# Kernel tuning notes

Measured on AMD Instinct MI355X. Metric: run time of the kernel, lower is better.

The kernel has to match this reference:

```python
import jax, jax.numpy as jnp
import numpy as np

NUM_HEAD = 12
D_MODEL = 768
SEQ_LEN = 4096
D_K = D_MODEL // NUM_HEAD
NEG = -1e9  # matches masked_fill(-1000000000.0)


def setup_inputs() -> dict:
    key = jax.random.key(0)
    ks = jax.random.split(key, 9)
    s = 1.0 / np.sqrt(D_MODEL)
    inp = {
        "x": jax.random.normal(ks[0], (1, SEQ_LEN, D_MODEL), jnp.float32),
        "Wq": jax.random.normal(ks[1], (D_MODEL, D_MODEL), jnp.float32) * s,
        "bq": jax.random.normal(ks[2], (D_MODEL,), jnp.float32) * 0.01,
        "Wk": jax.random.normal(ks[3], (D_MODEL, D_MODEL), jnp.float32) * s,
        "bk": jax.random.normal(ks[4], (D_MODEL,), jnp.float32) * 0.01,
        "Wv": jax.random.normal(ks[5], (D_MODEL, D_MODEL), jnp.float32) * s,
        "bv": jax.random.normal(ks[6], (D_MODEL,), jnp.float32) * 0.01,
        "Wo": jax.random.normal(ks[7], (D_MODEL, D_MODEL), jnp.float32) * s,
        "bo": jax.random.normal(ks[8], (D_MODEL,), jnp.float32) * 0.01,
    }
    return inp


def reference(x, Wq, bq, Wk, bk, Wv, bv, Wo, bo):
    # x: [B, S, D]. nn.Linear computes x @ W.T + b.
    B, S, D = x.shape

    def proj(W, b):
        y = jnp.einsum("bsd,ed->bse", x, W) + b
        # [B, S, H, d_k] -> [B, H, S, d_k]
        return y.reshape(B, S, NUM_HEAD, D_K).transpose(0, 2, 1, 3)

    q = proj(Wq, bq)
    k = proj(Wk, bk)
    v = proj(Wv, bv)

    scores = jnp.einsum("bhqd,bhkd->bhqk", q, k) / jnp.sqrt(
        jnp.asarray(D_K, x.dtype)
    )
    # causal (subsequent) mask: position q attends to k <= q
    causal = jnp.tril(jnp.ones((S, S), bool))
    scores = jnp.where(causal[None, None], scores, jnp.asarray(NEG, x.dtype))
    p_attn = jax.nn.softmax(scores, axis=-1)  # dropout is identity in eval
    ctx = jnp.einsum("bhqk,bhkd->bhqd", p_attn, v)
    ctx = ctx.transpose(0, 2, 1, 3).reshape(B, S, D)
    return jnp.einsum("bsd,ed->bse", ctx, Wo) + bo
```

## Files before the change

kernel.cpp:

```cpp
#include <hip/hip_runtime.h>

#define SEQ 4096
#define DM  768
#define NH  12
#define DK  64

typedef __bf16 bf16_t;
typedef bf16_t bf16x8 __attribute__((ext_vector_type(8)));
typedef bf16_t bf16x4 __attribute__((ext_vector_type(4)));
typedef float  f32x4  __attribute__((ext_vector_type(4)));
typedef short  s16x4  __attribute__((ext_vector_type(4)));

#define LOG2E 1.44269504088896340736f
#define SM_C  16.0f

static __device__ inline f32x4 mfma16x16x16_bf16(bf16x4 a, bf16x4 b, f32x4 c) {
#if __has_builtin(__builtin_amdgcn_mfma_f32_16x16x16_bf16)
    return __builtin_amdgcn_mfma_f32_16x16x16_bf16(a, b, c, 0, 0, 0);
#else
    return __builtin_amdgcn_mfma_f32_16x16x16bf16_1k(
        __builtin_bit_cast(s16x4, a), __builtin_bit_cast(s16x4, b), c, 0, 0, 0);
#endif
}

__global__ __launch_bounds__(256) void gemm_qkv(
    const float* __restrict__ x,
    const float* __restrict__ Wq, const float* __restrict__ bq,
    const float* __restrict__ Wk, const float* __restrict__ bk,
    const float* __restrict__ Wv, const float* __restrict__ bv,
    bf16_t* __restrict__ Qb, bf16_t* __restrict__ Kb, bf16_t* __restrict__ Vbt)
{
    const float* W; const float* bias;
    if (blockIdx.z == 0)      { W = Wq; bias = bq; }
    else if (blockIdx.z == 1) { W = Wk; bias = bk; }
    else                      { W = Wv; bias = bv; }

    __shared__ bf16_t As[128][40];
    __shared__ bf16_t Bs[128][40];

    const int tid  = threadIdx.x;
    const int wave = tid >> 6;
    const int lane = tid & 63;
    const int wm   = wave & 1, wn = wave >> 1;
    const int lrow = lane & 15;
    const int quad = lane >> 4;
    const int row0 = blockIdx.x * 128;
    const int col0 = blockIdx.y * 128;

    f32x4 acc[4][4];
    #pragma unroll
    for (int i = 0; i < 4; i++)
        #pragma unroll
        for (int j = 0; j < 4; j++)
            acc[i][j] = (f32x4){0.f, 0.f, 0.f, 0.f};

    for (int k0 = 0; k0 < DM; k0 += 32) {
        __syncthreads();
        #pragma unroll
        for (int i = 0; i < 4; i++) {
            int v  = tid + i * 256;
            int r  = v >> 3;
            int c4 = v & 7;
            float4 av = *(const float4*)&x[(size_t)(row0 + r) * DM + k0 + c4 * 4];
            bf16x4 at;
            at[0] = (bf16_t)av.x; at[1] = (bf16_t)av.y;
            at[2] = (bf16_t)av.z; at[3] = (bf16_t)av.w;
            *(bf16x4*)&As[r][c4 * 4] = at;
            float4 bv4 = *(const float4*)&W[(size_t)(col0 + r) * DM + k0 + c4 * 4];
            bf16x4 bt;
            bt[0] = (bf16_t)bv4.x; bt[1] = (bf16_t)bv4.y;
            bt[2] = (bf16_t)bv4.z; bt[3] = (bf16_t)bv4.w;
            *(bf16x4*)&Bs[r][c4 * 4] = bt;
        }
        __syncthreads();

        bf16x8 afrag[4], bfrag[4];
        #pragma unroll
        for (int mt = 0; mt < 4; mt++)
            afrag[mt] = *(const bf16x8*)&As[wm * 64 + mt * 16 + lrow][quad * 8];
        #pragma unroll
        for (int nt = 0; nt < 4; nt++)
            bfrag[nt] = *(const bf16x8*)&Bs[wn * 64 + nt * 16 + lrow][quad * 8];
        #pragma unroll
        for (int mt = 0; mt < 4; mt++)
            #pragma unroll
            for (int nt = 0; nt < 4; nt++)
                acc[mt][nt] = __builtin_amdgcn_mfma_f32_16x16x32_bf16(
                    afrag[mt], bfrag[nt], acc[mt][nt], 0, 0, 0);
    }

    if (blockIdx.z == 2) {
        #pragma unroll
        for (int nt = 0; nt < 4; nt++) {
            int col = col0 + wn * 64 + nt * 16 + lrow;
            float bv = bias[col];
            #pragma unroll
            for (int mt = 0; mt < 4; mt++) {
                int row = row0 + wm * 64 + mt * 16 + quad * 4;
                bf16x4 t;
                #pragma unroll
                for (int r = 0; r < 4; r++) t[r] = (bf16_t)(acc[mt][nt][r] + bv);
                *(bf16x4*)&Vbt[(size_t)col * SEQ + row] = t;
            }
        }
    } else {
        bf16_t* Cout = (blockIdx.z == 0) ? Qb : Kb;
        #pragma unroll
        for (int nt = 0; nt < 4; nt++) {
            int col = col0 + wn * 64 + nt * 16 + lrow;
            float bv = bias[col];
            #pragma unroll
            for (int mt = 0; mt < 4; mt++) {
                #pragma unroll
                for (int r = 0; r < 4; r++) {
                    int row = row0 + wm * 64 + mt * 16 + quad * 4 + r;
                    Cout[(size_t)row * DM + col] = (bf16_t)(acc[mt][nt][r] + bv);
                }
            }
        }
    }
}

__global__ __launch_bounds__(256) void gemm_out(
    const bf16_t* __restrict__ A, const float* __restrict__ W,
    const float* __restrict__ bias, float* __restrict__ C)
{
    __shared__ bf16_t As[128][40];
    __shared__ bf16_t Bs[128][40];

    const int tid  = threadIdx.x;
    const int wave = tid >> 6;
    const int lane = tid & 63;
    const int wm   = wave & 1, wn = wave >> 1;
    const int lrow = lane & 15;
    const int quad = lane >> 4;
    const int row0 = blockIdx.x * 128;
    const int col0 = blockIdx.y * 128;

    f32x4 acc[4][4];
    #pragma unroll
    for (int i = 0; i < 4; i++)
        #pragma unroll
        for (int j = 0; j < 4; j++)
            acc[i][j] = (f32x4){0.f, 0.f, 0.f, 0.f};

    for (int k0 = 0; k0 < DM; k0 += 32) {
        __syncthreads();
        #pragma unroll
        for (int i = 0; i < 2; i++) {
            int v  = tid + i * 256;
            int r  = v >> 2;
            int c8 = v & 3;
            *(bf16x8*)&As[r][c8 * 8] =
                *(const bf16x8*)&A[(size_t)(row0 + r) * DM + k0 + c8 * 8];
        }
        #pragma unroll
        for (int i = 0; i < 4; i++) {
            int v  = tid + i * 256;
            int r  = v >> 3;
            int c4 = v & 7;
            float4 bv4 = *(const float4*)&W[(size_t)(col0 + r) * DM + k0 + c4 * 4];
            bf16x4 bt;
            bt[0] = (bf16_t)bv4.x; bt[1] = (bf16_t)bv4.y;
            bt[2] = (bf16_t)bv4.z; bt[3] = (bf16_t)bv4.w;
            *(bf16x4*)&Bs[r][c4 * 4] = bt;
        }
        __syncthreads();

        bf16x8 afrag[4], bfrag[4];
        #pragma unroll
        for (int mt = 0; mt < 4; mt++)
            afrag[mt] = *(const bf16x8*)&As[wm * 64 + mt * 16 + lrow][quad * 8];
        #pragma unroll
        for (int nt = 0; nt < 4; nt++)
            bfrag[nt] = *(const bf16x8*)&Bs[wn * 64 + nt * 16 + lrow][quad * 8];
        #pragma unroll
        for (int mt = 0; mt < 4; mt++)
            #pragma unroll
            for (int nt = 0; nt < 4; nt++)
                acc[mt][nt] = __builtin_amdgcn_mfma_f32_16x16x32_bf16(
                    afrag[mt], bfrag[nt], acc[mt][nt], 0, 0, 0);
    }

    #pragma unroll
    for (int nt = 0; nt < 4; nt++) {
        int col = col0 + wn * 64 + nt * 16 + lrow;
        float bv = bias[col];
        #pragma unroll
        for (int mt = 0; mt < 4; mt++) {
            #pragma unroll
            for (int r = 0; r < 4; r++) {
                int row = row0 + wm * 64 + mt * 16 + quad * 4 + r;
                C[(size_t)row * DM + col] = acc[mt][nt][r] + bv;
            }
        }
    }
}

__global__ __launch_bounds__(256) void flash_attn(
    const bf16_t* __restrict__ Qb, const bf16_t* __restrict__ Kb,
    const bf16_t* __restrict__ Vbt, bf16_t* __restrict__ Ctx)
{
    const int qi   = gridDim.x - 1 - blockIdx.x;
    const int h    = blockIdx.y;
    const int tid  = threadIdx.x;
    const int wave = tid >> 6;
    const int lane = tid & 63;
    const int lrow = lane & 15;
    const int quad = lane >> 4;
    const int q0   = qi * 64;

    __shared__ bf16_t Ks[64][72];
    __shared__ bf16_t Vt[64][76];

    const int qrow = q0 + wave * 16 + lrow;
    bf16x8 qfrag[2];
    #pragma unroll
    for (int s = 0; s < 2; s++) {
        bf16x8 t = *(const bf16x8*)&Qb[(size_t)qrow * DM + h * DK + s * 32 + quad * 8];
        #pragma unroll
        for (int j = 0; j < 8; j++)
            t[j] = (bf16_t)((float)t[j] * 0.125f);
        qfrag[s] = t;
    }

    f32x4 oT[4];
    #pragma unroll
    for (int dt = 0; dt < 4; dt++) oT[dt] = (f32x4){0.f, 0.f, 0.f, 0.f};
    float l_i = 0.f;

    const int r0 = tid >> 3;
    const int c0 = (tid & 7) * 8;

    const bf16_t* Kbase = Kb  + (size_t)h * DK + c0;
    const bf16_t* Vbase = Vbt + (size_t)(h * DK) * SEQ + c0;

    bf16x8 kr0 = *(const bf16x8*)&Kbase[(size_t)(r0)      * DM];
    bf16x8 kr1 = *(const bf16x8*)&Kbase[(size_t)(r0 + 32) * DM];
    bf16x8 vr0 = *(const bf16x8*)&Vbase[(size_t)(r0)      * SEQ];
    bf16x8 vr1 = *(const bf16x8*)&Vbase[(size_t)(r0 + 32) * SEQ];

    for (int kt = 0; kt <= qi; kt++) {
        __syncthreads();
        *(bf16x8*)&Ks[r0][c0]      = kr0;
        *(bf16x8*)&Ks[r0 + 32][c0] = kr1;
        *(bf16x8*)&Vt[r0][c0]      = vr0;
        *(bf16x8*)&Vt[r0 + 32][c0] = vr1;
        __syncthreads();

        if (kt < qi) {
            size_t ko = (size_t)(kt + 1) * 64;
            kr0 = *(const bf16x8*)&Kbase[(ko + r0)      * DM];
            kr1 = *(const bf16x8*)&Kbase[(ko + r0 + 32) * DM];
            vr0 = *(const bf16x8*)&Vbase[(size_t)(r0)      * SEQ + ko];
            vr1 = *(const bf16x8*)&Vbase[(size_t)(r0 + 32) * SEQ + ko];
        }

        f32x4 sc[4];
        #pragma unroll
        for (int mt = 0; mt < 4; mt++) {
            f32x4 a = (f32x4){0.f, 0.f, 0.f, 0.f};
            #pragma unroll
            for (int s = 0; s < 2; s++) {
                bf16x8 kf = *(const bf16x8*)&Ks[mt * 16 + lrow][s * 32 + quad * 8];
                a = __builtin_amdgcn_mfma_f32_16x16x32_bf16(kf, qfrag[s], a, 0, 0, 0);
            }
            sc[mt] = a;
        }

        if (kt == qi) {
            int lq = wave * 16 + lrow;
            #pragma unroll
            for (int mt = 0; mt < 4; mt++)
                #pragma unroll
                for (int r = 0; r < 4; r++)
                    if (mt * 16 + quad * 4 + r > lq) sc[mt][r] = -1e30f;
        }

        bf16x4 pf[4];
        float rsum = 0.f;
        #pragma unroll
        for (int mt = 0; mt < 4; mt++) {
            bf16x4 t;
            #pragma unroll
            for (int r = 0; r < 4; r++) {
                float p = __builtin_amdgcn_exp2f((sc[mt][r] - SM_C) * LOG2E);
                rsum += p;
                t[r] = (bf16_t)p;
            }
            pf[mt] = t;
        }
        l_i += rsum;

        #pragma unroll
        for (int dt = 0; dt < 4; dt++)
            #pragma unroll
            for (int kb = 0; kb < 4; kb++) {
                bf16x4 vf = *(const bf16x4*)&Vt[dt * 16 + lrow][kb * 16 + quad * 4];
                oT[dt] = mfma16x16x16_bf16(vf, pf[kb], oT[dt]);
            }
    }

    l_i += __shfl_xor(l_i, 16, 64);
    l_i += __shfl_xor(l_i, 32, 64);
    float inv_l = 1.f / l_i;
    #pragma unroll
    for (int dt = 0; dt < 4; dt++) {
        bf16x4 ov;
        #pragma unroll
        for (int r = 0; r < 4; r++) ov[r] = (bf16_t)(oT[dt][r] * inv_l);
        *(bf16x4*)&Ctx[(size_t)(q0 + wave * 16 + lrow) * DM
                       + h * DK + dt * 16 + quad * 4] = ov;
    }
}

extern "C" void kernel_launch(void* const* d_in, const int* in_sizes, int n_in,
                              void* d_out, int out_size, void* d_ws, size_t ws_size,
                              hipStream_t stream) {
    const float* x  = (const float*)d_in[0];
    const float* Wq = (const float*)d_in[1];
    const float* bq = (const float*)d_in[2];
    const float* Wk = (const float*)d_in[3];
    const float* bk = (const float*)d_in[4];
    const float* Wv = (const float*)d_in[5];
    const float* bv = (const float*)d_in[6];
    const float* Wo = (const float*)d_in[7];
    const float* bo = (const float*)d_in[8];
    float* out = (float*)d_out;

    bf16_t* Qb  = (bf16_t*)d_ws;
    bf16_t* Kb  = Qb  + (size_t)SEQ * DM;
    bf16_t* Vbt = Kb  + (size_t)SEQ * DM;
    bf16_t* Cx  = Vbt + (size_t)SEQ * DM;

    dim3 g1(SEQ / 128, DM / 128, 3);
    gemm_qkv<<<g1, 256, 0, stream>>>(x, Wq, bq, Wk, bk, Wv, bv, Qb, Kb, Vbt);

    dim3 g2(SEQ / 64, NH);
    flash_attn<<<g2, 256, 0, stream>>>(Qb, Kb, Vbt, Cx);

    dim3 g3(SEQ / 128, DM / 128);
    gemm_out<<<g3, 256, 0, stream>>>(Cx, Wo, bo, out);
}
```

Measured before the change: 232.3 us.

## Pre-convert to bf16, use direct LDS loads, and split attention over key chunks

Adds a conversion kernel that turns x and all weights into bf16 once, so the GEMMs can stream bf16 through global_load_lds into XOR-swizzled 64-wide K tiles. The attention kernel is split along the key axis into up to four 16-tile chunks with double-buffered LDS and no per-tile barrier pair; partial outputs and row sums are accumulated with float atomics, then normalized and transposed in a new epilogue kernel. The Q scale moves into K's projection epilogue, and the output GEMM uses 128x64 tiles for more blocks. The split is meant to fix load imbalance from the causal triangle, but it adds a memset, atomic traffic, a fixed softmax offset shared across chunks, and two extra launches.

```diff
diff --git a/kernel.cpp b/kernel.cpp
--- a/kernel.cpp
+++ b/kernel.cpp
@@ -23,20 +23,48 @@
 #endif
 }
 
-__global__ __launch_bounds__(256) void gemm_qkv(
-    const float* __restrict__ x,
-    const float* __restrict__ Wq, const float* __restrict__ bq,
-    const float* __restrict__ Wk, const float* __restrict__ bk,
-    const float* __restrict__ Wv, const float* __restrict__ bv,
+static __device__ __forceinline__ void gl_lds16(const bf16_t* g, bf16_t* l) {
+    __builtin_amdgcn_global_load_lds(
+        (const __attribute__((address_space(1))) void*)g,
+        (__attribute__((address_space(3))) void*)l, 16, 0, 0);
+}
+
+__global__ __launch_bounds__(256) void cvt_bf16(
+    const float* __restrict__ x,  const float* __restrict__ Wq,
+    const float* __restrict__ Wk, const float* __restrict__ Wv,
+    const float* __restrict__ Wo,
+    bf16_t* __restrict__ xb, bf16_t* __restrict__ Wb)
+{
+    const int NXV = SEQ * DM / 4;
+    const int NWV = DM * DM / 4;
+    int i4 = blockIdx.x * 256 + threadIdx.x;
+    const float* src; bf16_t* dst; int off;
+    if (i4 < NXV) { src = x; dst = xb; off = i4; }
+    else {
+        int j = i4 - NXV;
+        int w = j / NWV, jj = j - w * NWV;
+        src = (w == 0) ? Wq : (w == 1) ? Wk : (w == 2) ? Wv : Wo;
+        dst = Wb + (size_t)w * DM * DM;
+        off = jj;
+    }
+    float4 v = *(const float4*)&src[(size_t)off * 4];
+    bf16x4 t;
+    t[0] = (bf16_t)v.x; t[1] = (bf16_t)v.y; t[2] = (bf16_t)v.z; t[3] = (bf16_t)v.w;
+    *(bf16x4*)&dst[(size_t)off * 4] = t;
+}
+
+__global__ __launch_bounds__(256) void gemm_qkv2(
+    const bf16_t* __restrict__ A, const bf16_t* __restrict__ Wb,
+    const float* __restrict__ bq, const float* __restrict__ bk,
+    const float* __restrict__ bv,
     bf16_t* __restrict__ Qb, bf16_t* __restrict__ Kb, bf16_t* __restrict__ Vbt)
 {
-    const float* W; const float* bias;
-    if (blockIdx.z == 0)      { W = Wq; bias = bq; }
-    else if (blockIdx.z == 1) { W = Wk; bias = bk; }
-    else                      { W = Wv; bias = bv; }
-
-    __shared__ bf16_t As[128][40];
-    __shared__ bf16_t Bs[128][40];
+    const int z = blockIdx.z;
+    const bf16_t* W = Wb + (size_t)z * DM * DM;
+    const float* bias = (z == 0) ? bq : (z == 1) ? bk : bv;
+
+    __shared__ bf16_t As[128][64];
+    __shared__ bf16_t Bs[128][64];
 
     const int tid  = threadIdx.x;
     const int wave = tid >> 6;
@@ -47,6 +75,10 @@
     const int row0 = blockIdx.x * 128;
     const int col0 = blockIdx.y * 128;
 
+    const int srow   = lane >> 3;
+    const int schunk = (lane & 7) ^ srow;
+    const int swz    = lrow & 7;
+
     f32x4 acc[4][4];
     #pragma unroll
     for (int i = 0; i < 4; i++)
@@ -54,79 +86,78 @@
         for (int j = 0; j < 4; j++)
             acc[i][j] = (f32x4){0.f, 0.f, 0.f, 0.f};
 
-    for (int k0 = 0; k0 < DM; k0 += 32) {
+    for (int k0 = 0; k0 < DM; k0 += 64) {
         __syncthreads();
         #pragma unroll
-        for (int i = 0; i < 4; i++) {
-            int v  = tid + i * 256;
-            int r  = v >> 3;
-            int c4 = v & 7;
-            float4 av = *(const float4*)&x[(size_t)(row0 + r) * DM + k0 + c4 * 4];
-            bf16x4 at;
-            at[0] = (bf16_t)av.x; at[1] = (bf16_t)av.y;
-            at[2] = (bf16_t)av.z; at[3] = (bf16_t)av.w;
-            *(bf16x4*)&As[r][c4 * 4] = at;
-            float4 bv4 = *(const float4*)&W[(size_t)(col0 + r) * DM + k0 + c4 * 4];
-            bf16x4 bt;
-            bt[0] = (bf16_t)bv4.x; bt[1] = (bf16_t)bv4.y;
-            bt[2] = (bf16_t)bv4.z; bt[3] = (bf16_t)bv4.w;
-            *(bf16x4*)&Bs[r][c4 * 4] = bt;
+        for (int u = 0; u < 4; u++) {
+            int R0 = wave * 32 + u * 8;
+            gl_lds16(&A[(size_t)(row0 + R0 + srow) * DM + k0 + schunk * 8],
+                     &As[R0][0]);
+            gl_lds16(&W[(size_t)(col0 + R0 + srow) * DM + k0 + schunk * 8],
+                     &Bs[R0][0]);
         }
         __syncthreads();
 
-        bf16x8 afrag[4], bfrag[4];
-        #pragma unroll
-        for (int mt = 0; mt < 4; mt++)
-            afrag[mt] = *(const bf16x8*)&As[wm * 64 + mt * 16 + lrow][quad * 8];
-        #pragma unroll
-        for (int nt = 0; nt < 4; nt++)
-            bfrag[nt] = *(const bf16x8*)&Bs[wn * 64 + nt * 16 + lrow][quad * 8];
-        #pragma unroll
-        for (int mt = 0; mt < 4; mt++)
+        #pragma unroll
+        for (int s = 0; s < 2; s++) {
+            bf16x8 af[4], bfr[4];
+            #pragma unroll
+            for (int mt = 0; mt < 4; mt++)
+                af[mt] = *(const bf16x8*)
+                    &As[wm * 64 + mt * 16 + lrow][(((s << 2) | quad) ^ swz) * 8];
             #pragma unroll
             for (int nt = 0; nt < 4; nt++)
-                acc[mt][nt] = __builtin_amdgcn_mfma_f32_16x16x32_bf16(
-                    afrag[mt], bfrag[nt], acc[mt][nt], 0, 0, 0);
-    }
-
-    if (blockIdx.z == 2) {
+                bfr[nt] = *(const bf16x8*)
+                    &Bs[wn * 64 + nt * 16 + lrow][(((s << 2) | quad) ^ swz) * 8];
+            #pragma unroll
+            for (int mt = 0; mt < 4; mt++)
+                #pragma unroll
+                for (int nt = 0; nt < 4; nt++)
+                    acc[mt][nt] = __builtin_amdgcn_mfma_f32_16x16x32_bf16(
+                        af[mt], bfr[nt], acc[mt][nt], 0, 0, 0);
+        }
+    }
+
+    if (z == 2) {
         #pragma unroll
         for (int nt = 0; nt < 4; nt++) {
             int col = col0 + wn * 64 + nt * 16 + lrow;
-            float bv = bias[col];
+            float bvv = bias[col];
             #pragma unroll
             for (int mt = 0; mt < 4; mt++) {
                 int row = row0 + wm * 64 + mt * 16 + quad * 4;
                 bf16x4 t;
                 #pragma unroll
-                for (int r = 0; r < 4; r++) t[r] = (bf16_t)(acc[mt][nt][r] + bv);
+                for (int r = 0; r < 4; r++) t[r] = (bf16_t)(acc[mt][nt][r] + bvv);
                 *(bf16x4*)&Vbt[(size_t)col * SEQ + row] = t;
             }
         }
     } else {
-        bf16_t* Cout = (blockIdx.z == 0) ? Qb : Kb;
+        bf16_t* Cout = (z == 0) ? Qb : Kb;
+        float scale = (z == 1) ? 0.125f : 1.0f;
         #pragma unroll
         for (int nt = 0; nt < 4; nt++) {
             int col = col0 + wn * 64 + nt * 16 + lrow;
-            float bv = bias[col];
+            float bvv = bias[col];
             #pragma unroll
             for (int mt = 0; mt < 4; mt++) {
                 #pragma unroll
                 for (int r = 0; r < 4; r++) {
                     int row = row0 + wm * 64 + mt * 16 + quad * 4 + r;
-                    Cout[(size_t)row * DM + col] = (bf16_t)(acc[mt][nt][r] + bv);
+                    Cout[(size_t)row * DM + col] =
+                        (bf16_t)((acc[mt][nt][r] + bvv) * scale);
                 }
             }
         }
     }
 }
 
-__global__ __launch_bounds__(256) void gemm_out(
-    const bf16_t* __restrict__ A, const float* __restrict__ W,
+__global__ __launch_bounds__(256) void gemm_out2(
+    const bf16_t* __restrict__ A, const bf16_t* __restrict__ W,
     const float* __restrict__ bias, float* __restrict__ C)
 {
-    __shared__ bf16_t As[128][40];
-    __shared__ bf16_t Bs[128][40];
+    __shared__ bf16_t As[128][64];
+    __shared__ bf16_t Bs[64][64];
 
     const int tid  = threadIdx.x;
     const int wave = tid >> 6;
@@ -135,74 +166,81 @@
     const int lrow = lane & 15;
     const int quad = lane >> 4;
     const int row0 = blockIdx.x * 128;
-    const int col0 = blockIdx.y * 128;
-
-    f32x4 acc[4][4];
+    const int col0 = blockIdx.y * 64;
+
+    const int srow   = lane >> 3;
+    const int schunk = (lane & 7) ^ srow;
+    const int swz    = lrow & 7;
+
+    f32x4 acc[4][2];
     #pragma unroll
     for (int i = 0; i < 4; i++)
         #pragma unroll
-        for (int j = 0; j < 4; j++)
+        for (int j = 0; j < 2; j++)
             acc[i][j] = (f32x4){0.f, 0.f, 0.f, 0.f};
 
-    for (int k0 = 0; k0 < DM; k0 += 32) {
+    for (int k0 = 0; k0 < DM; k0 += 64) {
         __syncthreads();
         #pragma unroll
-        for (int i = 0; i < 2; i++) {
-            int v  = tid + i * 256;
-            int r  = v >> 2;
-            int c8 = v & 3;
-            *(bf16x8*)&As[r][c8 * 8] =
-                *(const bf16x8*)&A[(size_t)(row0 + r) * DM + k0 + c8 * 8];
-        }
-        #pragma unroll
-        for (int i = 0; i < 4; i++) {
-            int v  = tid + i * 256;
-            int r  = v >> 3;
-            int c4 = v & 7;
-            float4 bv4 = *(const float4*)&W[(size_t)(col0 + r) * DM + k0 + c4 * 4];
-            bf16x4 bt;
-            bt[0] = (bf16_t)bv4.x; bt[1] = (bf16_t)bv4.y;
-            bt[2] = (bf16_t)bv4.z; bt[3] = (bf16_t)bv4.w;
-            *(bf16x4*)&Bs[r][c4 * 4] = bt;
+        for (int u = 0; u < 4; u++) {
+            int R0 = wave * 32 + u * 8;
+            gl_lds16(&A[(size_t)(row0 + R0 + srow) * DM + k0 + schunk * 8],
+                     &As[R0][0]);
+        }
+        #pragma unroll
+        for (int u = 0; u < 2; u++) {
+            int R0 = wave * 16 + u * 8;
+            gl_lds16(&W[(size_t)(col0 + R0 + srow) * DM + k0 + schunk * 8],
+                     &Bs[R0][0]);
         }
         __syncthreads();
 
-        bf16x8 afrag[4], bfrag[4];
-        #pragma unroll
-        for (int mt = 0; mt < 4; mt++)
-            afrag[mt] = *(const bf16x8*)&As[wm * 64 + mt * 16 + lrow][quad * 8];
-        #pragma unroll
-        for (int nt = 0; nt < 4; nt++)
-            bfrag[nt] = *(const bf16x8*)&Bs[wn * 64 + nt * 16 + lrow][quad * 8];
-        #pragma unroll
-        for (int mt = 0; mt < 4; mt++)
-            #pragma unroll
-            for (int nt = 0; nt < 4; nt++)
-                acc[mt][nt] = __builtin_amdgcn_mfma_f32_16x16x32_bf16(
-                    afrag[mt], bfrag[nt], acc[mt][nt], 0, 0, 0);
-    }
-
-    #pragma unroll
-    for (int nt = 0; nt < 4; nt++) {
-        int col = col0 + wn * 64 + nt * 16 + lrow;
-        float bv = bias[col];
+        #pragma unroll
+        for (int s = 0; s < 2; s++) {
+            bf16x8 af[4], bfr[2];
+            #pragma unroll
+            for (int mt = 0; mt < 4; mt++)
+                af[mt] = *(const bf16x8*)
+                    &As[wm * 64 + mt * 16 + lrow][(((s << 2) | quad) ^ swz) * 8];
+            #pragma unroll
+            for (int nt = 0; nt < 2; nt++)
+                bfr[nt] = *(const bf16x8*)
+                    &Bs[wn * 32 + nt * 16 + lrow][(((s << 2) | quad) ^ swz) * 8];
+            #pragma unroll
+            for (int mt = 0; mt < 4; mt++)
+                #pragma unroll
+                for (int nt = 0; nt < 2; nt++)
+                    acc[mt][nt] = __builtin_amdgcn_mfma_f32_16x16x32_bf16(
+                        af[mt], bfr[nt], acc[mt][nt], 0, 0, 0);
+        }
+    }
+
+    #pragma unroll
+    for (int nt = 0; nt < 2; nt++) {
+        int col = col0 + wn * 32 + nt * 16 + lrow;
+        float bvv = bias[col];
         #pragma unroll
         for (int mt = 0; mt < 4; mt++) {
             #pragma unroll
             for (int r = 0; r < 4; r++) {
                 int row = row0 + wm * 64 + mt * 16 + quad * 4 + r;
-                C[(size_t)row * DM + col] = acc[mt][nt][r] + bv;
-            }
-        }
-    }
-}
-
-__global__ __launch_bounds__(256) void flash_attn(
+                C[(size_t)row * DM + col] = acc[mt][nt][r] + bvv;
+            }
+        }
+    }
+}
+
+__global__ __launch_bounds__(256) void flash_split2(
     const bf16_t* __restrict__ Qb, const bf16_t* __restrict__ Kb,
-    const bf16_t* __restrict__ Vbt, bf16_t* __restrict__ Ctx)
+    const bf16_t* __restrict__ Vbt,
+    float* __restrict__ Oacc ,
+    float* __restrict__ Lacc )
 {
-    const int qi   = gridDim.x - 1 - blockIdx.x;
-    const int h    = blockIdx.y;
+    const int qi = blockIdx.x;
+    const int s0 = blockIdx.y * 16;
+    if (s0 > qi) return;
+    const int h    = blockIdx.z;
+    const int kend = min(s0 + 15, qi);
     const int tid  = threadIdx.x;
     const int wave = tid >> 6;
     const int lane = tid & 63;
@@ -210,19 +248,14 @@
     const int quad = lane >> 4;
     const int q0   = qi * 64;
 
-    __shared__ bf16_t Ks[64][72];
-    __shared__ bf16_t Vt[64][76];
+    __shared__ bf16_t Ks[2][64][72];
+    __shared__ bf16_t Vt[2][64][76];
 
     const int qrow = q0 + wave * 16 + lrow;
     bf16x8 qfrag[2];
     #pragma unroll
-    for (int s = 0; s < 2; s++) {
-        bf16x8 t = *(const bf16x8*)&Qb[(size_t)qrow * DM + h * DK + s * 32 + quad * 8];
-        #pragma unroll
-        for (int j = 0; j < 8; j++)
-            t[j] = (bf16_t)((float)t[j] * 0.125f);
-        qfrag[s] = t;
-    }
+    for (int s = 0; s < 2; s++)
+        qfrag[s] = *(const bf16x8*)&Qb[(size_t)qrow * DM + h * DK + s * 32 + quad * 8];
 
     f32x4 oT[4];
     #pragma unroll
@@ -231,29 +264,29 @@
 
     const int r0 = tid >> 3;
     const int c0 = (tid & 7) * 8;
-
     const bf16_t* Kbase = Kb  + (size_t)h * DK + c0;
     const bf16_t* Vbase = Vbt + (size_t)(h * DK) * SEQ + c0;
 
-    bf16x8 kr0 = *(const bf16x8*)&Kbase[(size_t)(r0)      * DM];
-    bf16x8 kr1 = *(const bf16x8*)&Kbase[(size_t)(r0 + 32) * DM];
-    bf16x8 vr0 = *(const bf16x8*)&Vbase[(size_t)(r0)      * SEQ];
-    bf16x8 vr1 = *(const bf16x8*)&Vbase[(size_t)(r0 + 32) * SEQ];
-
-    for (int kt = 0; kt <= qi; kt++) {
+    size_t ko = (size_t)s0 * 64;
+    bf16x8 kr0 = *(const bf16x8*)&Kbase[(ko + r0)      * DM];
+    bf16x8 kr1 = *(const bf16x8*)&Kbase[(ko + r0 + 32) * DM];
+    bf16x8 vr0 = *(const bf16x8*)&Vbase[(size_t)(r0)      * SEQ + ko];
+    bf16x8 vr1 = *(const bf16x8*)&Vbase[(size_t)(r0 + 32) * SEQ + ko];
+
+    for (int kt = s0; kt <= kend; kt++) {
+        const int b = kt & 1;
+        *(bf16x8*)&Ks[b][r0][c0]      = kr0;
+        *(bf16x8*)&Ks[b][r0 + 32][c0] = kr1;
+        *(bf16x8*)&Vt[b][r0][c0]      = vr0;
+        *(bf16x8*)&Vt[b][r0 + 32][c0] = vr1;
         __syncthreads();
-        *(bf16x8*)&Ks[r0][c0]      = kr0;
-        *(bf16x8*)&Ks[r0 + 32][c0] = kr1;
-        *(bf16x8*)&Vt[r0][c0]      = vr0;
-        *(bf16x8*)&Vt[r0 + 32][c0] = vr1;
-        __syncthreads();
-
-        if (kt < qi) {
-            size_t ko = (size_t)(kt + 1) * 64;
-            kr0 = *(const bf16x8*)&Kbase[(ko + r0)      * DM];
-            kr1 = *(const bf16x8*)&Kbase[(ko + r0 + 32) * DM];
-            vr0 = *(const bf16x8*)&Vbase[(size_t)(r0)      * SEQ + ko];
-            vr1 = *(const bf16x8*)&Vbase[(size_t)(r0 + 32) * SEQ + ko];
+
+        if (kt < kend) {
+            size_t kn = (size_t)(kt + 1) * 64;
+            kr0 = *(const bf16x8*)&Kbase[(kn + r0)      * DM];
+            kr1 = *(const bf16x8*)&Kbase[(kn + r0 + 32) * DM];
+            vr0 = *(const bf16x8*)&Vbase[(size_t)(r0)      * SEQ + kn];
+            vr1 = *(const bf16x8*)&Vbase[(size_t)(r0 + 32) * SEQ + kn];
         }
 
         f32x4 sc[4];
@@ -262,7 +295,7 @@
             f32x4 a = (f32x4){0.f, 0.f, 0.f, 0.f};
             #pragma unroll
             for (int s = 0; s < 2; s++) {
-                bf16x8 kf = *(const bf16x8*)&Ks[mt * 16 + lrow][s * 32 + quad * 8];
+                bf16x8 kf = *(const bf16x8*)&Ks[b][mt * 16 + lrow][s * 32 + quad * 8];
                 a = __builtin_amdgcn_mfma_f32_16x16x32_bf16(kf, qfrag[s], a, 0, 0, 0);
             }
             sc[mt] = a;
@@ -296,21 +329,56 @@
         for (int dt = 0; dt < 4; dt++)
             #pragma unroll
             for (int kb = 0; kb < 4; kb++) {
-                bf16x4 vf = *(const bf16x4*)&Vt[dt * 16 + lrow][kb * 16 + quad * 4];
+                bf16x4 vf = *(const bf16x4*)&Vt[b][dt * 16 + lrow][kb * 16 + quad * 4];
                 oT[dt] = mfma16x16x16_bf16(vf, pf[kb], oT[dt]);
             }
     }
 
+    #pragma unroll
+    for (int dt = 0; dt < 4; dt++)
+        #pragma unroll
+        for (int r = 0; r < 4; r++) {
+            int d = dt * 16 + quad * 4 + r;
+            atomicAdd(&Oacc[((size_t)h * DK + d) * SEQ + q0 + wave * 16 + lrow],
+                      oT[dt][r]);
+        }
     l_i += __shfl_xor(l_i, 16, 64);
     l_i += __shfl_xor(l_i, 32, 64);
-    float inv_l = 1.f / l_i;
-    #pragma unroll
-    for (int dt = 0; dt < 4; dt++) {
-        bf16x4 ov;
-        #pragma unroll
-        for (int r = 0; r < 4; r++) ov[r] = (bf16_t)(oT[dt][r] * inv_l);
-        *(bf16x4*)&Ctx[(size_t)(q0 + wave * 16 + lrow) * DM
-                       + h * DK + dt * 16 + quad * 4] = ov;
+    if (quad == 0)
+        atomicAdd(&Lacc[(size_t)h * SEQ + qrow], l_i);
+}
+
+__global__ __launch_bounds__(256) void ctx_epilogue(
+    const float* __restrict__ Oacc, const float* __restrict__ Lacc,
+    bf16_t* __restrict__ Ctx)
+{
+    const int qt = blockIdx.x;
+    const int h  = blockIdx.y;
+    const int tid = threadIdx.x;
+    __shared__ float T[64][65];
+
+    #pragma unroll
+    for (int i = 0; i < 4; i++) {
+        int v  = tid + i * 256;
+        int d  = v >> 4;
+        int qv = v & 15;
+        f32x4 o4 = *(const f32x4*)&Oacc[((size_t)h * DK + d) * SEQ + qt * 64 + qv * 4];
+        f32x4 l4 = *(const f32x4*)&Lacc[(size_t)h * SEQ + qt * 64 + qv * 4];
+        #pragma unroll
+        for (int j = 0; j < 4; j++)
+            T[qv * 4 + j][d] = o4[j] / l4[j];
+    }
+    __syncthreads();
+    #pragma unroll
+    for (int i = 0; i < 2; i++) {
+        int v  = tid + i * 256;
+        int q  = v >> 3;
+        int c8 = v & 7;
+        bf16x8 t;
+        #pragma unroll
+        for (int j = 0; j < 8; j++)
+            t[j] = (bf16_t)T[q][c8 * 8 + j];
+        *(bf16x8*)&Ctx[(size_t)(qt * 64 + q) * DM + h * DK + c8 * 8] = t;
     }
 }
 
@@ -328,17 +396,31 @@
     const float* bo = (const float*)d_in[8];
     float* out = (float*)d_out;
 
-    bf16_t* Qb  = (bf16_t*)d_ws;
-    bf16_t* Kb  = Qb  + (size_t)SEQ * DM;
-    bf16_t* Vbt = Kb  + (size_t)SEQ * DM;
-    bf16_t* Cx  = Vbt + (size_t)SEQ * DM;
+    const size_t NX = (size_t)SEQ * DM;
+    const size_t NW = (size_t)DM * DM;
+
+    bf16_t* xb   = (bf16_t*)d_ws;
+    bf16_t* Qb   = xb  + NX;
+    bf16_t* Kb   = Qb  + NX;
+    bf16_t* Vbt  = Kb  + NX;
+    bf16_t* Wb   = Vbt + NX;
+    float*  Oacc = (float*)(Wb + 4 * NW);
+    float*  Lacc = Oacc + NX;
+    bf16_t* Cx   = xb;
+
+    int cvt_blocks = (int)((NX + 4 * NW) / 4 / 256);
+    cvt_bf16<<<cvt_blocks, 256, 0, stream>>>(x, Wq, Wk, Wv, Wo, xb, Wb);
+    hipMemsetAsync(Oacc, 0, (NX + (size_t)NH * SEQ) * 4, stream);
 
     dim3 g1(SEQ / 128, DM / 128, 3);
-    gemm_qkv<<<g1, 256, 0, stream>>>(x, Wq, bq, Wk, bk, Wv, bv, Qb, Kb, Vbt);
-
-    dim3 g2(SEQ / 64, NH);
-    flash_attn<<<g2, 256, 0, stream>>>(Qb, Kb, Vbt, Cx);
-
-    dim3 g3(SEQ / 128, DM / 128);
-    gemm_out<<<g3, 256, 0, stream>>>(Cx, Wo, bo, out);
-}
+    gemm_qkv2<<<g1, 256, 0, stream>>>(xb, Wb, bq, bk, bv, Qb, Kb, Vbt);
+
+    dim3 g2(SEQ / 64, 4, NH);
+    flash_split2<<<g2, 256, 0, stream>>>(Qb, Kb, Vbt, Oacc, Lacc);
+
+    dim3 g3(SEQ / 64, NH);
+    ctx_epilogue<<<g3, 256, 0, stream>>>(Oacc, Lacc, Cx);
+
+    dim3 g4(SEQ / 128, DM / 64);
+    gemm_out2<<<g4, 256, 0, stream>>>(Cx, Wb + 3 * NW, bo, out);
+}
```

Result: faster. 200.9 us (-13.5%).
